# Performance work log

Hardware: AMD Instinct MI355X
Metric: run time of the kernel (lower is better)

Reference implementation:

```python
import jax, jax.numpy as jnp
import numpy as np

BS = 16384
NUM_ALLY, NUM_ADV, NUM_LM = 3, 2, 3
ALLY_D, ADV_D, LM_D = 4, 4, 2
HEAD, HID, HYPER = 4, 64, 64
OUT = HEAD * HID  # 256


def _lin_init(key, fan_in, fan_out):
    k1, k2 = jax.random.split(key)
    s = 1.0 / np.sqrt(fan_in)
    W = jax.random.uniform(k1, (fan_in, fan_out), minval=-s, maxval=s, dtype=jnp.float32)
    b = jax.random.uniform(k2, (fan_out,), minval=-s, maxval=s, dtype=jnp.float32)
    return W, b


def setup_inputs() -> dict:
    key = jax.random.key(0)
    ks = jax.random.split(key, 12)
    inputs = jax.random.normal(ks[0], (BS, 30), dtype=jnp.float32)
    hidden_state = jnp.zeros((1, HID), dtype=jnp.float32)
    actions = jax.random.normal(ks[1], (BS, 2), dtype=jnp.float32)
    self_W, self_b = _lin_init(ks[2], 4, HID)
    ally_W1, ally_b1 = _lin_init(ks[3], ALLY_D, HYPER)
    ally_W2, ally_b2 = _lin_init(ks[4], HYPER, (ALLY_D + 1) * OUT)
    adv_W1, adv_b1 = _lin_init(ks[5], ADV_D, HYPER)
    adv_W2, adv_b2 = _lin_init(ks[6], HYPER, (ADV_D + 1) * OUT)
    lm_W1, lm_b1 = _lin_init(ks[7], LM_D, HYPER)
    lm_W2, lm_b2 = _lin_init(ks[8], HYPER, (LM_D + 1) * OUT)
    merger_w = jnp.ones((1, HEAD, HID), dtype=jnp.float32)
    fc1_W, fc1_b = _lin_init(ks[9], HID + 2, HID)
    fc2_W, fc2_b = _lin_init(ks[10], HID, 1)
    return dict(inputs=inputs, hidden_state=hidden_state, actions=actions,
                self_W=self_W, self_b=self_b,
                ally_W1=ally_W1, ally_b1=ally_b1, ally_W2=ally_W2, ally_b2=ally_b2,
                adv_W1=adv_W1, adv_b1=adv_b1, adv_W2=adv_W2, adv_b2=adv_b2,
                lm_W1=lm_W1, lm_b1=lm_b1, lm_W2=lm_W2, lm_b2=lm_b2,
                merger_w=merger_w, fc1_W=fc1_W, fc1_b=fc1_b, fc2_W=fc2_W, fc2_b=fc2_b)


def _split_obs(ob):
    self_feats = ob[:, :4]
    i1 = 4 + NUM_LM * LM_D
    lm = ob[:, 4:i1].reshape(-1, NUM_LM, LM_D)
    i2 = i1 + NUM_ALLY * 2
    ally_pos = ob[:, i1:i2].reshape(-1, NUM_ALLY, 2)
    i3 = i2 + NUM_ADV * 2
    adv_pos = ob[:, i2:i3].reshape(-1, NUM_ADV, 2)
    i4 = i3 + NUM_ALLY * 2
    ally_vel = ob[:, i3:i4].reshape(-1, NUM_ALLY, 2)
    i5 = i4 + NUM_ADV * 2
    adv_vel = ob[:, i4:i5].reshape(-1, NUM_ADV, 2)
    ally = jnp.concatenate([ally_pos, ally_vel], axis=-1)
    adv = jnp.concatenate([adv_pos, adv_vel], axis=-1)
    return self_feats, ally, adv, lm


def _branch(feats, W1, b1, W2, b2, d, n):
    # feats: [bs, n, d] -> per-entity hypernet weight [d, HEAD*HID] and bias
    h = jax.nn.leaky_relu(feats @ W1 + b1, negative_slope=0.01)
    out = h @ W2 + b2                              # [bs, n, (d+1)*256]
    w = out[..., :d * OUT].reshape(-1, d, OUT)     # [bs*n, d, 256]
    b = out[..., d * OUT:].reshape(-1, 1, OUT)     # [bs*n, 1, 256]
    y = jnp.matmul(feats.reshape(-1, 1, d), w) + b # [bs*n, 1, 256]
    return y.reshape(-1, n, HEAD, HID).sum(axis=1) # [bs, HEAD, HID]


def reference(inputs, hidden_state, actions,
              self_W, self_b,
              ally_W1, ally_b1, ally_W2, ally_b2,
              adv_W1, adv_b1, adv_W2, adv_b2,
              lm_W1, lm_b1, lm_W2, lm_b2,
              merger_w, fc1_W, fc1_b, fc2_W, fc2_b):
    self_feats, ally_feats, adv_feats, lm_feats = _split_obs(inputs)
    self_out = self_feats @ self_W + self_b                       # [bs, 64]
    ally_out = _branch(ally_feats, ally_W1, ally_b1, ally_W2, ally_b2, ALLY_D, NUM_ALLY)
    adv_out = _branch(adv_feats, adv_W1, adv_b1, adv_W2, adv_b2, ADV_D, NUM_ADV)
    lm_out = _branch(lm_feats, lm_W1, lm_b1, lm_W2, lm_b2, LM_D, NUM_LM)
    tmp = ally_out + lm_out + adv_out                             # [bs, 4, 64]
    merged = jnp.sum(jax.nn.softmax(merger_w, axis=1) * tmp, axis=1)
    out = jax.nn.relu(self_out + merged)
    out = jnp.concatenate([out, actions.reshape(-1, actions.shape[-1])], axis=-1)
    x = jax.nn.relu(out @ fc1_W + fc1_b)
    q = x @ fc2_W + fc2_b
    return q, x
```

## Files before the change

### kernel.cpp

```cpp
#include <hip/hip_runtime.h>

typedef __attribute__((ext_vector_type(8))) _Float16 f16x8;
typedef __attribute__((ext_vector_type(4))) float f32x4;

#define KTOT 864
#define FSTRIDE 872
#define OSTRIDE 104

__global__ __launch_bounds__(256) void precompute_kernel(
    const float* __restrict__ selfW, const float* __restrict__ selfB,
    const float* __restrict__ W2a, const float* __restrict__ b2a,
    const float* __restrict__ W2d, const float* __restrict__ b2d,
    const float* __restrict__ W2l, const float* __restrict__ b2l,
    const float* __restrict__ mergerW,
    const float* __restrict__ fc1W, const float* __restrict__ fc1b,
    _Float16* __restrict__ matB, _Float16* __restrict__ fc1B)
{
  int g = blockIdx.x * 256 + threadIdx.x;
  if (g < 64 * KTOT) {
    int j8 = g & 7;
    int l  = (g >> 3) & 63;
    int t  = g >> 9;
    int nt = t & 3, kk = t >> 2;
    int c  = nt * 16 + (l & 15);
    int k  = kk * 32 + (l >> 4) * 8 + j8;

    float v0 = mergerW[c], v1 = mergerW[64 + c], v2 = mergerW[128 + c], v3 = mergerW[192 + c];
    float mx = fmaxf(fmaxf(v0, v1), fmaxf(v2, v3));
    float e0 = expf(v0 - mx), e1 = expf(v1 - mx), e2 = expf(v2 - mx), e3 = expf(v3 - mx);
    float inv = 1.f / (e0 + e1 + e2 + e3);
    float w0 = e0 * inv, w1 = e1 * inv, w2 = e2 * inv, w3 = e3 * inv;
    auto HS = [&](const float* __restrict__ p, int base) -> float {
      return w0 * p[base + c] + w1 * p[base + 64 + c] + w2 * p[base + 128 + c] + w3 * p[base + 192 + c];
    };
    float val = 0.f;
    if (k < 256)      { int kkk = k >> 6, j = k & 63;             val = HS(W2a, j * 1280 + kkk * 256); }
    else if (k < 320) { int j = k - 256;                          val = HS(W2a, j * 1280 + 1024); }
    else if (k < 324) { int kkk = k - 320;                        val = HS(b2a, kkk * 256); }
    else if (k < 580) { int k2 = k - 324; int kkk = k2 >> 6, j = k2 & 63; val = HS(W2d, j * 1280 + kkk * 256); }
    else if (k < 644) { int j = k - 580;                          val = HS(W2d, j * 1280 + 1024); }
    else if (k < 648) { int kkk = k - 644;                        val = HS(b2d, kkk * 256); }
    else if (k < 776) { int k2 = k - 648; int kkk = k2 >> 6, j = k2 & 63; val = HS(W2l, j * 768 + kkk * 256); }
    else if (k < 840) { int j = k - 776;                          val = HS(W2l, j * 768 + 512); }
    else if (k < 842) { int kkk = k - 840;                        val = HS(b2l, kkk * 256); }
    else if (k < 846) {                                           val = selfW[(k - 842) * 64 + c]; }
    else if (k == 846){ val = 3.f * HS(b2a, 1024) + 2.f * HS(b2d, 1024) + 3.f * HS(b2l, 512) + selfB[c]; }
    matB[g] = (_Float16)val;
  } else {
    int g2 = g - 64 * KTOT;
    int j8 = g2 & 7;
    int l  = (g2 >> 3) & 63;
    int t  = g2 >> 9;
    int nt = t & 3, kk = t >> 2;
    int c  = nt * 16 + (l & 15);
    int k  = kk * 32 + (l >> 4) * 8 + j8;
    float val = 0.f;
    if (k < 66)       val = fc1W[k * 64 + c];
    else if (k == 66) val = fc1b[c];
    fc1B[g2] = (_Float16)val;
  }
}

__global__ __launch_bounds__(64) void hpn_main(
    const float* __restrict__ inputs, const float* __restrict__ actions,
    const float* __restrict__ W1a, const float* __restrict__ B1a,
    const float* __restrict__ W1d, const float* __restrict__ B1d,
    const float* __restrict__ W1l, const float* __restrict__ B1l,
    const _Float16* __restrict__ matB, const _Float16* __restrict__ fc1B,
    const float* __restrict__ fc2W, const float* __restrict__ fc2b,
    float* __restrict__ q_out, float* __restrict__ x_out)
{
  __shared__ __align__(16) float   stage[16 * 32];
  __shared__ __align__(16) _Float16 feats[16 * FSTRIDE];
  __shared__ __align__(16) _Float16 outact[16 * OSTRIDE];

  const int lane = threadIdx.x;
  const int base = blockIdx.x * 16;
  const int m = lane & 15;
  const int quad = lane >> 4;

  float sbuf[8];
#pragma unroll
  for (int c = 0; c < 8; ++c) {
    int idx = lane + c * 64;
    int row = idx >> 5, col = idx & 31;
    sbuf[c] = (col < 30) ? inputs[(base + row) * 30 + col] : 0.f;
  }
  float a0 = 0.f, a1 = 0.f;
  if (lane < 16) { a0 = actions[base * 2 + 2 * lane]; a1 = actions[base * 2 + 2 * lane + 1]; }

  float w1a0 = W1a[lane], w1a1 = W1a[64 + lane], w1a2 = W1a[128 + lane], w1a3 = W1a[192 + lane];
  float vb1a = B1a[lane];
  float w1d0 = W1d[lane], w1d1 = W1d[64 + lane], w1d2 = W1d[128 + lane], w1d3 = W1d[192 + lane];
  float vb1d = B1d[lane];
  float w1l0 = W1l[lane], w1l1 = W1l[64 + lane];
  float vb1l = B1l[lane];

  float wq0 = fc2W[m], wq1 = fc2W[16 + m], wq2 = fc2W[32 + m], wq3 = fc2W[48 + m];
  float qb = fc2b[0];

  const _Float16* bbase = matB + lane * 8;
  f16x8 b0 = *(const f16x8*)(bbase);
  f16x8 b1 = *(const f16x8*)(bbase + 512);
  f16x8 b2 = *(const f16x8*)(bbase + 1024);
  f16x8 b3 = *(const f16x8*)(bbase + 1536);

  const _Float16* cbase = fc1B + lane * 8;
  f16x8 cfrag[12];
#pragma unroll
  for (int t = 0; t < 12; ++t) cfrag[t] = *(const f16x8*)(cbase + t * 512);

#pragma unroll
  for (int c = 0; c < 8; ++c) stage[lane + c * 64] = sbuf[c];
#pragma unroll
  for (int p = 0; p < 4; ++p) {
    int idx = p * 64 + lane;
    int row = idx >> 4, d = idx & 15;
    *(float*)(feats + row * FSTRIDE + 832 + d * 2) = 0.f;
  }
#pragma unroll
  for (int p = 0; p < 4; ++p) {
    int idx = p * 64 + lane;
    int row = idx >> 4, d = idx & 15;
    *(float*)(outact + row * OSTRIDE + 64 + d * 2) = 0.f;
  }

  for (int i = 0; i < 16; ++i) {
    float r[30];
#pragma unroll
    for (int e = 0; e < 30; ++e) r[e] = stage[i * 32 + e];
    _Float16* fr = feats + i * FSTRIDE;

    float Ua0 = 0, Ua1 = 0, Ua2 = 0, Ua3 = 0, hsa = 0;
#pragma unroll
    for (int n = 0; n < 3; ++n) {
      float f0 = r[10 + 2 * n], f1 = r[11 + 2 * n];
      float f2 = r[20 + 2 * n], f3 = r[21 + 2 * n];
      float t = fmaf(f0, w1a0, fmaf(f1, w1a1, fmaf(f2, w1a2, fmaf(f3, w1a3, vb1a))));
      float h = t > 0.f ? t : 0.01f * t;
      Ua0 = fmaf(h, f0, Ua0); Ua1 = fmaf(h, f1, Ua1);
      Ua2 = fmaf(h, f2, Ua2); Ua3 = fmaf(h, f3, Ua3); hsa += h;
    }
    fr[lane] = (_Float16)Ua0; fr[64 + lane] = (_Float16)Ua1;
    fr[128 + lane] = (_Float16)Ua2; fr[192 + lane] = (_Float16)Ua3;
    fr[256 + lane] = (_Float16)hsa;

    float Ud0 = 0, Ud1 = 0, Ud2 = 0, Ud3 = 0, hsd = 0;
#pragma unroll
    for (int n = 0; n < 2; ++n) {
      float f0 = r[16 + 2 * n], f1 = r[17 + 2 * n];
      float f2 = r[26 + 2 * n], f3 = r[27 + 2 * n];
      float t = fmaf(f0, w1d0, fmaf(f1, w1d1, fmaf(f2, w1d2, fmaf(f3, w1d3, vb1d))));
      float h = t > 0.f ? t : 0.01f * t;
      Ud0 = fmaf(h, f0, Ud0); Ud1 = fmaf(h, f1, Ud1);
      Ud2 = fmaf(h, f2, Ud2); Ud3 = fmaf(h, f3, Ud3); hsd += h;
    }
    fr[324 + lane] = (_Float16)Ud0; fr[388 + lane] = (_Float16)Ud1;
    fr[452 + lane] = (_Float16)Ud2; fr[516 + lane] = (_Float16)Ud3;
    fr[580 + lane] = (_Float16)hsd;

    float Ul0 = 0, Ul1 = 0, hsl = 0;
#pragma unroll
    for (int n = 0; n < 3; ++n) {
      float f0 = r[4 + 2 * n], f1 = r[5 + 2 * n];
      float t = fmaf(f0, w1l0, fmaf(f1, w1l1, vb1l));
      float h = t > 0.f ? t : 0.01f * t;
      Ul0 = fmaf(h, f0, Ul0); Ul1 = fmaf(h, f1, Ul1); hsl += h;
    }
    fr[648 + lane] = (_Float16)Ul0; fr[712 + lane] = (_Float16)Ul1;
    fr[776 + lane] = (_Float16)hsl;
  }

#pragma unroll
  for (int p = 0; p < 4; ++p) {
    int idx = p * 64 + lane;
    int i = idx >> 4, t = idx & 15;
    const float* rs = stage + i * 32;
    float val;
    if (t < 4)       { int b = ((t < 2) ? 10 : 20) + (t & 1); val = rs[b] + rs[b + 2] + rs[b + 4]; }
    else if (t < 8)  { int b = ((t < 6) ? 16 : 26) + (t & 1); val = rs[b] + rs[b + 2]; }
    else if (t < 10) { int b = 4 + (t & 1);                   val = rs[b] + rs[b + 2] + rs[b + 4]; }
    else if (t < 14) {                                        val = rs[t - 10]; }
    else if (t == 14){                                        val = 1.0f; }
    else             {                                        val = 0.0f; }
    int k = (t < 4) ? 320 + t : (t < 8) ? 640 + t : (t < 15) ? 832 + t : 863;
    feats[i * FSTRIDE + k] = (_Float16)val;
  }

  f32x4 acc[4];
#pragma unroll
  for (int nt = 0; nt < 4; ++nt) acc[nt] = (f32x4){0.f, 0.f, 0.f, 0.f};

  const _Float16* aptr = feats + m * FSTRIDE + quad * 8;
  {
    f16x8 af = *(const f16x8*)(aptr);
    acc[0] = __builtin_amdgcn_mfma_f32_16x16x32_f16(af, b0, acc[0], 0, 0, 0);
    acc[1] = __builtin_amdgcn_mfma_f32_16x16x32_f16(af, b1, acc[1], 0, 0, 0);
    acc[2] = __builtin_amdgcn_mfma_f32_16x16x32_f16(af, b2, acc[2], 0, 0, 0);
    acc[3] = __builtin_amdgcn_mfma_f32_16x16x32_f16(af, b3, acc[3], 0, 0, 0);
  }
#pragma unroll 3
  for (int kk = 1; kk < 27; ++kk) {
    f16x8 af = *(const f16x8*)(aptr + kk * 32);
#pragma unroll
    for (int nt = 0; nt < 4; ++nt) {
      f16x8 bf = *(const f16x8*)(bbase + (kk * 4 + nt) * 512);
      acc[nt] = __builtin_amdgcn_mfma_f32_16x16x32_f16(af, bf, acc[nt], 0, 0, 0);
    }
  }

#pragma unroll
  for (int nt = 0; nt < 4; ++nt)
#pragma unroll
    for (int i = 0; i < 4; ++i) {
      int rrow = quad * 4 + i;
      float v = fmaxf(acc[nt][i], 0.f);
      outact[rrow * OSTRIDE + nt * 16 + m] = (_Float16)v;
    }
  if (lane < 16) {
    _Float16* orp = outact + lane * OSTRIDE;
    orp[64] = (_Float16)a0;
    orp[65] = (_Float16)a1;
    orp[66] = (_Float16)1.0f;
  }

  f32x4 xacc[4];
#pragma unroll
  for (int nt = 0; nt < 4; ++nt) xacc[nt] = (f32x4){0.f, 0.f, 0.f, 0.f};
  const _Float16* aptr2 = outact + m * OSTRIDE + quad * 8;
#pragma unroll
  for (int kk = 0; kk < 3; ++kk) {
    f16x8 af = *(const f16x8*)(aptr2 + kk * 32);
#pragma unroll
    for (int nt = 0; nt < 4; ++nt)
      xacc[nt] = __builtin_amdgcn_mfma_f32_16x16x32_f16(af, cfrag[kk * 4 + nt], xacc[nt], 0, 0, 0);
  }

#pragma unroll
  for (int i = 0; i < 4; ++i) {
    int rrow = quad * 4 + i;
    int s = base + rrow;
    float x0 = fmaxf(xacc[0][i], 0.f);
    float x1 = fmaxf(xacc[1][i], 0.f);
    float x2 = fmaxf(xacc[2][i], 0.f);
    float x3 = fmaxf(xacc[3][i], 0.f);
    x_out[s * 64 + m]      = x0;
    x_out[s * 64 + 16 + m] = x1;
    x_out[s * 64 + 32 + m] = x2;
    x_out[s * 64 + 48 + m] = x3;
    float p = fmaf(x0, wq0, fmaf(x1, wq1, fmaf(x2, wq2, x3 * wq3)));
    p += __shfl_xor(p, 1, 64);
    p += __shfl_xor(p, 2, 64);
    p += __shfl_xor(p, 4, 64);
    p += __shfl_xor(p, 8, 64);
    if (m == 0) q_out[s] = p + qb;
  }
}

extern "C" void kernel_launch(void* const* d_in, const int* in_sizes, int n_in,
                              void* d_out, int out_size, void* d_ws, size_t ws_size,
                              hipStream_t stream) {
  const float* inputs  = (const float*)d_in[0];
  const float* actions = (const float*)d_in[2];
  const float* selfW   = (const float*)d_in[3];
  const float* selfB   = (const float*)d_in[4];
  const float* W1a = (const float*)d_in[5],  *B1a = (const float*)d_in[6];
  const float* W2a = (const float*)d_in[7],  *b2a = (const float*)d_in[8];
  const float* W1d = (const float*)d_in[9],  *B1d = (const float*)d_in[10];
  const float* W2d = (const float*)d_in[11], *b2d = (const float*)d_in[12];
  const float* W1l = (const float*)d_in[13], *B1l = (const float*)d_in[14];
  const float* W2l = (const float*)d_in[15], *b2l = (const float*)d_in[16];
  const float* mergerW = (const float*)d_in[17];
  const float* fc1W = (const float*)d_in[18], *fc1b = (const float*)d_in[19];
  const float* fc2W = (const float*)d_in[20], *fc2b = (const float*)d_in[21];

  _Float16* matB = (_Float16*)d_ws;
  _Float16* fc1B = matB + 64 * KTOT;

  const int n = in_sizes[0] / 30;
  precompute_kernel<<<240, 256, 0, stream>>>(selfW, selfB, W2a, b2a, W2d, b2d,
                                             W2l, b2l, mergerW, fc1W, fc1b,
                                             matB, fc1B);
  float* q_out = (float*)d_out;
  float* x_out = q_out + n;
  hpn_main<<<n / 16, 64, 0, stream>>>(inputs, actions, W1a, B1a, W1d, B1d,
                                      W1l, B1l, matB, fc1B, fc2W, fc2b,
                                      q_out, x_out);
}
```

Measured before the change: 111.8 us.

## Split hypernetwork GEMM K-range across two waves with LDS partial reduction

The main kernel now launches 128 threads per block instead of 64. Each wave builds features for 8 of the 16 rows and computes half of the 27-step K loop (13 and 14 steps), then wave 1 writes its partial accumulators to LDS and wave 0 adds them before the fc1/fc2 epilogue. The feature layout is permuted so the per-entity products are stored as packed fp16 pairs via cvt_pkrtz, and the precomputed weight matrix is reordered to match. This aims to raise parallelism and shorten the serial per-block chain, at the cost of two barriers, extra LDS, and an idle second wave during the epilogue.

```diff
diff --git a/kernel.cpp b/kernel.cpp
--- a/kernel.cpp
+++ b/kernel.cpp
@@ -34,13 +34,13 @@
       return w0 * p[base + c] + w1 * p[base + 64 + c] + w2 * p[base + 128 + c] + w3 * p[base + 192 + c];
     };
     float val = 0.f;
-    if (k < 256)      { int kkk = k >> 6, j = k & 63;             val = HS(W2a, j * 1280 + kkk * 256); }
+    if (k < 256)      { int j = k >> 2, kkk = k & 3;              val = HS(W2a, j * 1280 + kkk * 256); }
     else if (k < 320) { int j = k - 256;                          val = HS(W2a, j * 1280 + 1024); }
     else if (k < 324) { int kkk = k - 320;                        val = HS(b2a, kkk * 256); }
-    else if (k < 580) { int k2 = k - 324; int kkk = k2 >> 6, j = k2 & 63; val = HS(W2d, j * 1280 + kkk * 256); }
+    else if (k < 580) { int k2 = k - 324; int j = k2 >> 2, kkk = k2 & 3; val = HS(W2d, j * 1280 + kkk * 256); }
     else if (k < 644) { int j = k - 580;                          val = HS(W2d, j * 1280 + 1024); }
     else if (k < 648) { int kkk = k - 644;                        val = HS(b2d, kkk * 256); }
-    else if (k < 776) { int k2 = k - 648; int kkk = k2 >> 6, j = k2 & 63; val = HS(W2l, j * 768 + kkk * 256); }
+    else if (k < 776) { int k2 = k - 648; int j = k2 >> 1, kkk = k2 & 1; val = HS(W2l, j * 768 + kkk * 256); }
     else if (k < 840) { int j = k - 776;                          val = HS(W2l, j * 768 + 512); }
     else if (k < 842) { int kkk = k - 840;                        val = HS(b2l, kkk * 256); }
     else if (k < 846) {                                           val = selfW[(k - 842) * 64 + c]; }
@@ -61,7 +61,7 @@
   }
 }
 
-__global__ __launch_bounds__(64) void hpn_main(
+__global__ __launch_bounds__(128) void hpn_main(
     const float* __restrict__ inputs, const float* __restrict__ actions,
     const float* __restrict__ W1a, const float* __restrict__ B1a,
     const float* __restrict__ W1d, const float* __restrict__ B1d,
@@ -70,24 +70,27 @@
     const float* __restrict__ fc2W, const float* __restrict__ fc2b,
     float* __restrict__ q_out, float* __restrict__ x_out)
 {
-  __shared__ __align__(16) float   stage[16 * 32];
+  __shared__ __align__(16) float    stage[16 * 32];
   __shared__ __align__(16) _Float16 feats[16 * FSTRIDE];
   __shared__ __align__(16) _Float16 outact[16 * OSTRIDE];
-
-  const int lane = threadIdx.x;
+  __shared__ __align__(16) float    partial[64 * 16];
+
+  const int tid  = threadIdx.x;
+  const int lane = tid & 63;
+  const int wave = tid >> 6;
   const int base = blockIdx.x * 16;
   const int m = lane & 15;
   const int quad = lane >> 4;
 
-  float sbuf[8];
-#pragma unroll
-  for (int c = 0; c < 8; ++c) {
+  float sbuf[4];
+#pragma unroll
+  for (int c = 0; c < 4; ++c) {
     int idx = lane + c * 64;
-    int row = idx >> 5, col = idx & 31;
+    int row = wave * 8 + (idx >> 5), col = idx & 31;
     sbuf[c] = (col < 30) ? inputs[(base + row) * 30 + col] : 0.f;
   }
   float a0 = 0.f, a1 = 0.f;
-  if (lane < 16) { a0 = actions[base * 2 + 2 * lane]; a1 = actions[base * 2 + 2 * lane + 1]; }
+  if (tid < 16) { a0 = actions[base * 2 + 2 * tid]; a1 = actions[base * 2 + 2 * tid + 1]; }
 
   float w1a0 = W1a[lane], w1a1 = W1a[64 + lane], w1a2 = W1a[128 + lane], w1a3 = W1a[192 + lane];
   float vb1a = B1a[lane];
@@ -100,32 +103,32 @@
   float qb = fc2b[0];
 
   const _Float16* bbase = matB + lane * 8;
-  f16x8 b0 = *(const f16x8*)(bbase);
-  f16x8 b1 = *(const f16x8*)(bbase + 512);
-  f16x8 b2 = *(const f16x8*)(bbase + 1024);
-  f16x8 b3 = *(const f16x8*)(bbase + 1536);
-
-  const _Float16* cbase = fc1B + lane * 8;
-  f16x8 cfrag[12];
-#pragma unroll
-  for (int t = 0; t < 12; ++t) cfrag[t] = *(const f16x8*)(cbase + t * 512);
-
-#pragma unroll
-  for (int c = 0; c < 8; ++c) stage[lane + c * 64] = sbuf[c];
-#pragma unroll
-  for (int p = 0; p < 4; ++p) {
+  const int kk0 = wave * 13;
+  f16x8 bp[4];
+#pragma unroll
+  for (int nt = 0; nt < 4; ++nt) bp[nt] = *(const f16x8*)(bbase + (kk0 * 4 + nt) * 512);
+
+#pragma unroll
+  for (int c = 0; c < 4; ++c) {
+    int idx = lane + c * 64;
+    int row = wave * 8 + (idx >> 5), col = idx & 31;
+    stage[row * 32 + col] = sbuf[c];
+  }
+#pragma unroll
+  for (int p = 0; p < 2; ++p) {
     int idx = p * 64 + lane;
-    int row = idx >> 4, d = idx & 15;
+    int row = wave * 8 + (idx >> 4), d = idx & 15;
     *(float*)(feats + row * FSTRIDE + 832 + d * 2) = 0.f;
   }
 #pragma unroll
-  for (int p = 0; p < 4; ++p) {
-    int idx = p * 64 + lane;
+  for (int p = 0; p < 2; ++p) {
+    int idx = p * 128 + tid;
     int row = idx >> 4, d = idx & 15;
     *(float*)(outact + row * OSTRIDE + 64 + d * 2) = 0.f;
   }
 
-  for (int i = 0; i < 16; ++i) {
+  for (int ii = 0; ii < 8; ++ii) {
+    int i = wave * 8 + ii;
     float r[30];
 #pragma unroll
     for (int e = 0; e < 30; ++e) r[e] = stage[i * 32 + e];
@@ -141,9 +144,13 @@
       Ua0 = fmaf(h, f0, Ua0); Ua1 = fmaf(h, f1, Ua1);
       Ua2 = fmaf(h, f2, Ua2); Ua3 = fmaf(h, f3, Ua3); hsa += h;
     }
-    fr[lane] = (_Float16)Ua0; fr[64 + lane] = (_Float16)Ua1;
-    fr[128 + lane] = (_Float16)Ua2; fr[192 + lane] = (_Float16)Ua3;
-    fr[256 + lane] = (_Float16)hsa;
+    {
+      auto p0 = __builtin_amdgcn_cvt_pkrtz(Ua0, Ua1);
+      auto p1 = __builtin_amdgcn_cvt_pkrtz(Ua2, Ua3);
+      *(decltype(p0)*)(fr + 4 * lane) = p0;
+      *(decltype(p1)*)(fr + 4 * lane + 2) = p1;
+      fr[256 + lane] = (_Float16)hsa;
+    }
 
     float Ud0 = 0, Ud1 = 0, Ud2 = 0, Ud3 = 0, hsd = 0;
 #pragma unroll
@@ -155,9 +162,13 @@
       Ud0 = fmaf(h, f0, Ud0); Ud1 = fmaf(h, f1, Ud1);
       Ud2 = fmaf(h, f2, Ud2); Ud3 = fmaf(h, f3, Ud3); hsd += h;
     }
-    fr[324 + lane] = (_Float16)Ud0; fr[388 + lane] = (_Float16)Ud1;
-    fr[452 + lane] = (_Float16)Ud2; fr[516 + lane] = (_Float16)Ud3;
-    fr[580 + lane] = (_Float16)hsd;
+    {
+      auto p0 = __builtin_amdgcn_cvt_pkrtz(Ud0, Ud1);
+      auto p1 = __builtin_amdgcn_cvt_pkrtz(Ud2, Ud3);
+      *(decltype(p0)*)(fr + 324 + 4 * lane) = p0;
+      *(decltype(p1)*)(fr + 324 + 4 * lane + 2) = p1;
+      fr[580 + lane] = (_Float16)hsd;
+    }
 
     float Ul0 = 0, Ul1 = 0, hsl = 0;
 #pragma unroll
@@ -167,14 +178,17 @@
       float h = t > 0.f ? t : 0.01f * t;
       Ul0 = fmaf(h, f0, Ul0); Ul1 = fmaf(h, f1, Ul1); hsl += h;
     }
-    fr[648 + lane] = (_Float16)Ul0; fr[712 + lane] = (_Float16)Ul1;
-    fr[776 + lane] = (_Float16)hsl;
-  }
-
-#pragma unroll
-  for (int p = 0; p < 4; ++p) {
+    {
+      auto pl = __builtin_amdgcn_cvt_pkrtz(Ul0, Ul1);
+      *(decltype(pl)*)(fr + 648 + 2 * lane) = pl;
+      fr[776 + lane] = (_Float16)hsl;
+    }
+  }
+
+#pragma unroll
+  for (int p = 0; p < 2; ++p) {
     int idx = p * 64 + lane;
-    int i = idx >> 4, t = idx & 15;
+    int i = wave * 8 + (idx >> 4), t = idx & 15;
     const float* rs = stage + i * 32;
     float val;
     if (t < 4)       { int b = ((t < 2) ? 10 : 20) + (t & 1); val = rs[b] + rs[b + 2] + rs[b + 4]; }
@@ -187,20 +201,22 @@
     feats[i * FSTRIDE + k] = (_Float16)val;
   }
 
+  __syncthreads();
+
   f32x4 acc[4];
 #pragma unroll
   for (int nt = 0; nt < 4; ++nt) acc[nt] = (f32x4){0.f, 0.f, 0.f, 0.f};
 
   const _Float16* aptr = feats + m * FSTRIDE + quad * 8;
   {
-    f16x8 af = *(const f16x8*)(aptr);
-    acc[0] = __builtin_amdgcn_mfma_f32_16x16x32_f16(af, b0, acc[0], 0, 0, 0);
-    acc[1] = __builtin_amdgcn_mfma_f32_16x16x32_f16(af, b1, acc[1], 0, 0, 0);
-    acc[2] = __builtin_amdgcn_mfma_f32_16x16x32_f16(af, b2, acc[2], 0, 0, 0);
-    acc[3] = __builtin_amdgcn_mfma_f32_16x16x32_f16(af, b3, acc[3], 0, 0, 0);
-  }
+    f16x8 af = *(const f16x8*)(aptr + kk0 * 32);
+#pragma unroll
+    for (int nt = 0; nt < 4; ++nt)
+      acc[nt] = __builtin_amdgcn_mfma_f32_16x16x32_f16(af, bp[nt], acc[nt], 0, 0, 0);
+  }
+  const int kkend = kk0 + 13 + wave;
 #pragma unroll 3
-  for (int kk = 1; kk < 27; ++kk) {
+  for (int kk = kk0 + 1; kk < kkend; ++kk) {
     f16x8 af = *(const f16x8*)(aptr + kk * 32);
 #pragma unroll
     for (int nt = 0; nt < 4; ++nt) {
@@ -208,6 +224,26 @@
       acc[nt] = __builtin_amdgcn_mfma_f32_16x16x32_f16(af, bf, acc[nt], 0, 0, 0);
     }
   }
+
+  if (wave == 1) {
+#pragma unroll
+    for (int nt = 0; nt < 4; ++nt)
+#pragma unroll
+      for (int i = 0; i < 4; ++i)
+        partial[(nt * 4 + i) * 64 + lane] = acc[nt][i];
+  }
+  __syncthreads();
+  if (wave == 1) return;
+#pragma unroll
+  for (int nt = 0; nt < 4; ++nt)
+#pragma unroll
+    for (int i = 0; i < 4; ++i)
+      acc[nt][i] += partial[(nt * 4 + i) * 64 + lane];
+
+  const _Float16* cbase = fc1B + lane * 8;
+  f16x8 cfrag[12];
+#pragma unroll
+  for (int t = 0; t < 12; ++t) cfrag[t] = *(const f16x8*)(cbase + t * 512);
 
 #pragma unroll
   for (int nt = 0; nt < 4; ++nt)
@@ -283,7 +319,7 @@
                                              matB, fc1B);
   float* q_out = (float*)d_out;
   float* x_out = q_out + n;
-  hpn_main<<<n / 16, 64, 0, stream>>>(inputs, actions, W1a, B1a, W1d, B1d,
-                                      W1l, B1l, matB, fc1B, fc2W, fc2b,
-                                      q_out, x_out);
+  hpn_main<<<n / 16, 128, 0, stream>>>(inputs, actions, W1a, B1a, W1d, B1d,
+                                       W1l, B1l, matB, fc1B, fc2W, fc2b,
+                                       q_out, x_out);
 }
```

Result: faster. 109.1 us (-2.4%).
